# Kernel tuning notes

Measured on AMD Instinct MI355X. Metric: run time of the kernel, lower is better.

The kernel has to match this reference:

```python
import jax, jax.numpy as jnp
import numpy as np

B, R, IN_DIM = 32, 512, 1024
K, D = 4096, 256  # num_codebook_vectors, latent_dim
OUT_DIM = 1024
BETA = 0.25


def setup_inputs() -> dict:
    key = jax.random.key(0)
    ks = jax.random.split(key, 5)
    scale = 1.0 / K
    return {
        "z": jax.random.normal(ks[0], (B, R, IN_DIM), dtype=jnp.float32),
        "W_qa": jax.random.normal(ks[1], (IN_DIM, 2 * D), dtype=jnp.float32) * (IN_DIM ** -0.5),
        "b_qa": jnp.zeros((2 * D,), dtype=jnp.float32),
        "emb1": jax.random.uniform(ks[2], (K, D), dtype=jnp.float32, minval=-scale, maxval=scale),
        "emb2": jax.random.uniform(ks[3], (K, D), dtype=jnp.float32, minval=-scale, maxval=scale),
        "W_pq": jax.random.normal(ks[4], (2 * D, OUT_DIM), dtype=jnp.float32) * ((2 * D) ** -0.5),
        "b_pq": jnp.zeros((OUT_DIM,), dtype=jnp.float32),
    }


def _vq(z_h, emb):
    # z_h: [B, R, D], emb: [K, D]
    zf = z_h.reshape(-1, D)  # [N, D]
    # squared-distance matrix via GEMM: [N, K]
    d = (jnp.sum(zf * zf, axis=1, keepdims=True)
         + jnp.sum(emb * emb, axis=1)
         - 2.0 * zf @ emb.T)
    idx = jnp.argmin(d, axis=1)  # [N]
    z_q = emb[idx].reshape(z_h.shape)  # gather [B, R, D]
    enc_loss = jnp.mean((jax.lax.stop_gradient(z_q) - z_h) ** 2, axis=-1)
    code_loss = jnp.mean((z_q - jax.lax.stop_gradient(z_h)) ** 2, axis=-1)
    loss = enc_loss + BETA * code_loss  # [B, R]
    z_q_st = z_h + jax.lax.stop_gradient(z_q - z_h)  # straight-through
    return z_q_st, idx.reshape(z_h.shape[:2]), loss


def reference(z, W_qa, b_qa, emb1, emb2, W_pq, b_pq):
    h = z @ W_qa + b_qa  # [B, R, 2D]
    z1, z2 = h[..., :D], h[..., D:]
    zq1, idx1, loss1 = _vq(z1, emb1)
    zq2, idx2, loss2 = _vq(z2, emb2)
    loss = 0.5 * (loss1 + loss2)  # [B, R]
    z_q = jnp.concatenate([zq1, zq2], axis=-1) @ W_pq + b_pq  # [B, R, OUT_DIM]
    return z_q, idx1, idx2, loss
```

## Files before the change

### kernel.cpp

```cpp
#include <hip/hip_runtime.h>
#include <cstdint>
#include <cstddef>

#define MROWS 16384
#define INDIM 1024
#define DD    256
#define TWO_D 512
#define KC    4096
#define OUTD  1024
#define NZQ   (MROWS * OUTD)

typedef short bfrag __attribute__((ext_vector_type(8)));
typedef float ffrag __attribute__((ext_vector_type(4)));

__device__ __forceinline__ ushort f2bf(float f) {
    uint u = __float_as_uint(f);
    return (ushort)((u + 0x7FFFu + ((u >> 16) & 1u)) >> 16);
}

#define GLD16(dst, src)                                                        \
    __builtin_amdgcn_global_load_lds(                                          \
        (const __attribute__((address_space(1))) unsigned int*)(src),          \
        (__attribute__((address_space(3))) unsigned int*)(dst), 16, 0, 0)

__global__ __launch_bounds__(256) void k_gemm1(const float* __restrict__ z,
                                               const float* __restrict__ Wqa,
                                               const float* __restrict__ bqa,
                                               float* __restrict__ h,
                                               ushort* __restrict__ hbf) {
    __shared__ float As[2][128][16];
    __shared__ float Bs[2][16][128];
    const int tid = threadIdx.x;
    const int l = tid & 63, w = tid >> 6;
    const int tx = tid & 15, ty = tid >> 4;
    const int rb = blockIdx.x * 128;
    const int cb = blockIdx.y * 128;

    float acc[8][8] = {};

    const int sA = 4 * ((l & 3) ^ ((l >> 4) & 3));
    const float* aA0 = z + (size_t)(rb + 32 * w + (l >> 2)) * INDIM + sA;
    const float* aA1 = aA0 + (size_t)16 * INDIM;
    const float* bB0 = Wqa + (size_t)(4 * w + (l >> 5)) * TWO_D + cb + (l & 31) * 4;
    const float* bB1 = bB0 + (size_t)2 * TWO_D;

#define STAGE(buf, k0)                                                         \
    do {                                                                       \
        GLD16(&As[buf][32 * w][0],      aA0 + (k0));                           \
        GLD16(&As[buf][32 * w + 16][0], aA1 + (k0));                           \
        GLD16(&Bs[buf][4 * w][0],       bB0 + (size_t)(k0) * TWO_D);           \
        GLD16(&Bs[buf][4 * w + 2][0],   bB1 + (size_t)(k0) * TWO_D);           \
    } while (0)

    STAGE(0, 0);
    __syncthreads();

    const int xk = ty & 3;
    for (int t = 0; t < 64; ++t) {
        const int cur = t & 1;
        if (t < 63) STAGE(cur ^ 1, (t + 1) * 16);
        #pragma unroll
        for (int q = 0; q < 4; ++q) {
            float fa[8][4];
            #pragma unroll
            for (int i = 0; i < 4; ++i) {
                *reinterpret_cast<float4*>(&fa[i][0]) =
                    *reinterpret_cast<const float4*>(&As[cur][ty * 4 + i][(q ^ xk) * 4]);
                *reinterpret_cast<float4*>(&fa[4 + i][0]) =
                    *reinterpret_cast<const float4*>(&As[cur][64 + ty * 4 + i][(q ^ xk) * 4]);
            }
            #pragma unroll
            for (int c = 0; c < 4; ++c) {
                const int kk = q * 4 + c;
                float4 b0 = *reinterpret_cast<const float4*>(&Bs[cur][kk][tx * 4]);
                float4 b1 = *reinterpret_cast<const float4*>(&Bs[cur][kk][64 + tx * 4]);
                float bv[8] = {b0.x, b0.y, b0.z, b0.w, b1.x, b1.y, b1.z, b1.w};
                #pragma unroll
                for (int i = 0; i < 8; ++i)
                    #pragma unroll
                    for (int j = 0; j < 8; ++j)
                        acc[i][j] = fmaf(fa[i][c], bv[j], acc[i][j]);
            }
        }
        __syncthreads();
    }
#undef STAGE

    #pragma unroll
    for (int i = 0; i < 8; ++i) {
        const int row = rb + ((i < 4) ? (ty * 4 + i) : (64 + ty * 4 + i - 4));
        #pragma unroll
        for (int jh = 0; jh < 2; ++jh) {
            const int col = cb + jh * 64 + tx * 4;
            float v0 = acc[i][jh * 4 + 0] + bqa[col + 0];
            float v1 = acc[i][jh * 4 + 1] + bqa[col + 1];
            float v2 = acc[i][jh * 4 + 2] + bqa[col + 2];
            float v3 = acc[i][jh * 4 + 3] + bqa[col + 3];
            float4 vf = {v0, v1, v2, v3};
            *reinterpret_cast<float4*>(&h[(size_t)row * TWO_D + col]) = vf;
            ushort u[4] = {f2bf(v0), f2bf(v1), f2bf(v2), f2bf(v3)};
            *reinterpret_cast<uint2*>(&hbf[(size_t)row * TWO_D + col]) =
                *reinterpret_cast<uint2*>(u);
        }
    }
}

__global__ __launch_bounds__(256) void k_rnorm(const float* __restrict__ h,
                                               float* __restrict__ Rn) {
    const int wave = threadIdx.x >> 6;
    const int lane = threadIdx.x & 63;
    const int item = blockIdx.x * 4 + wave;
    const int row  = item & (MROWS - 1);
    const int half = item >> 14;
    float4 v = *reinterpret_cast<const float4*>(&h[(size_t)row * TWO_D + half * DD + lane * 4]);
    float s = v.x * v.x + v.y * v.y + v.z * v.z + v.w * v.w;
    #pragma unroll
    for (int off = 32; off; off >>= 1) s += __shfl_down(s, off, 64);
    if (lane == 0) Rn[half * MROWS + row] = s;
}

__global__ __launch_bounds__(256) void k_cvt(const float* __restrict__ e1,
                                             const float* __restrict__ e2,
                                             const float* __restrict__ Wpq,
                                             ushort* __restrict__ ebf,
                                             ushort* __restrict__ wbfT) {
    const int b = blockIdx.x;
    if (b < 2048) {
        const size_t v = ((size_t)b * 256 + threadIdx.x) * 4;
        const size_t half = (size_t)KC * DD;
        const float* src = (v < half) ? (e1 + v) : (e2 + (v - half));
        float4 f = *reinterpret_cast<const float4*>(src);
        ebf[v + 0] = f2bf(f.x); ebf[v + 1] = f2bf(f.y);
        ebf[v + 2] = f2bf(f.z); ebf[v + 3] = f2bf(f.w);
    } else {
        const int e = ((b - 2048) * 256 + threadIdx.x) * 4;
        const int k = e >> 10, c = e & 1023;
        float4 f = *reinterpret_cast<const float4*>(&Wpq[e]);
        wbfT[(size_t)(c + 0) * TWO_D + k] = f2bf(f.x);
        wbfT[(size_t)(c + 1) * TWO_D + k] = f2bf(f.y);
        wbfT[(size_t)(c + 2) * TWO_D + k] = f2bf(f.z);
        wbfT[(size_t)(c + 3) * TWO_D + k] = f2bf(f.w);
    }
}

__global__ __launch_bounds__(256) void k_score_mfma(const ushort* __restrict__ hbf,
                                                    const ushort* __restrict__ ebf,
                                                    uint* __restrict__ cand) {
    __shared__ ushort Ab[2][4][128][8];
    __shared__ ushort Bb[2][4][128][8];
    const int tid = threadIdx.x;
    const int l = tid & 63, w = tid >> 6;
    const int rb    = blockIdx.x * 128;
    const int cbcol = blockIdx.y * 128;
    const int cbk   = blockIdx.z;
    const ushort* hb = hbf + cbk * DD;
    const ushort* eb = ebf + (size_t)cbk * KC * DD;

    const int ry = (w & 1) * 64;
    const int cy = (w >> 1) * 64;

    const int koct = (w ^ ((l >> 1) & 3)) * 8;
    const ushort* aS0 = hb + (size_t)(rb + l) * TWO_D + koct;
    const ushort* aS1 = hb + (size_t)(rb + 64 + l) * TWO_D + koct;
    const ushort* bS0 = eb + (size_t)(cbcol + l) * DD + koct;
    const ushort* bS1 = eb + (size_t)(cbcol + 64 + l) * DD + koct;

#define SSTAGE(buf, k0)                                                        \
    do {                                                                       \
        GLD16(&Ab[buf][w][0][0],  aS0 + (k0));                                 \
        GLD16(&Ab[buf][w][64][0], aS1 + (k0));                                 \
        GLD16(&Bb[buf][w][0][0],  bS0 + (k0));                                 \
        GLD16(&Bb[buf][w][64][0], bS1 + (k0));                                 \
    } while (0)

    ffrag acc[4][4];
    #pragma unroll
    for (int i = 0; i < 4; ++i)
        #pragma unroll
        for (int j = 0; j < 4; ++j)
            acc[i][j] = (ffrag){0.f, 0.f, 0.f, 0.f};

    SSTAGE(0, 0);
    __syncthreads();

    const int q = l >> 4, li = l & 15;
    for (int c = 0; c < 8; ++c) {
        const int cur = c & 1;
        if (c < 7) SSTAGE(cur ^ 1, (c + 1) * 32);
        bfrag afr[4], bfr[4];
        #pragma unroll
        for (int rf = 0; rf < 4; ++rf) {
            const int r = ry + rf * 16 + li;
            afr[rf] = *reinterpret_cast<const bfrag*>(&Ab[cur][q ^ ((r >> 1) & 3)][r][0]);
        }
        #pragma unroll
        for (int cf = 0; cf < 4; ++cf) {
            const int cc = cy + cf * 16 + li;
            bfr[cf] = *reinterpret_cast<const bfrag*>(&Bb[cur][q ^ ((cc >> 1) & 3)][cc][0]);
        }
        #pragma unroll
        for (int rf = 0; rf < 4; ++rf)
            #pragma unroll
            for (int cf = 0; cf < 4; ++cf)
                acc[rf][cf] = __builtin_amdgcn_mfma_f32_16x16x32_bf16(afr[rf], bfr[cf],
                                                                      acc[rf][cf], 0, 0, 0);
        __syncthreads();
    }
#undef SSTAGE

    const int seg = blockIdx.y * 2 + (w >> 1);
    #pragma unroll
    for (int rf = 0; rf < 4; ++rf) {
        #pragma unroll
        for (int reg = 0; reg < 4; ++reg) {
            const int row = rb + ry + rf * 16 + q * 4 + reg;
            uint k1 = 0, k2 = 0;
            #pragma unroll
            for (int cf = 0; cf < 4; ++cf) {
                float v = acc[rf][cf][reg];
                const int code = cbcol + cy + cf * 16 + li;
                uint u = __float_as_uint(v);
                u ^= (0x80000000u | (uint)((int)u >> 31));
                const uint key = (u & 0xFFFFF000u) | (uint)code;
                if (key > k1) { k2 = k1; k1 = key; }
                else if (key > k2) { k2 = key; }
            }
            #pragma unroll
            for (int m = 1; m < 16; m <<= 1) {
                uint o1 = __shfl_xor((int)k1, m, 64);
                uint o2 = __shfl_xor((int)k2, m, 64);
                uint n1 = k1 > o1 ? k1 : o1;
                uint lo = k1 > o1 ? o1 : k1;
                uint hi2 = k2 > o2 ? k2 : o2;
                k2 = lo > hi2 ? lo : hi2;
                k1 = n1;
            }
            if (li == 0) {
                const size_t base = ((size_t)(cbk * 64 + seg) * MROWS + row) * 2;
                cand[base] = k1; cand[base + 1] = k2;
            }
        }
    }
}

__global__ __launch_bounds__(256) void k_reduce(const uint* __restrict__ cand,
                                                const float* __restrict__ h,
                                                const float* __restrict__ emb1,
                                                const float* __restrict__ emb2,
                                                const float* __restrict__ Rn,
                                                float* __restrict__ dout_idx) {
    const int tid = threadIdx.x;
    const int l = tid & 63, w = tid >> 6;
    const int item = blockIdx.x * 4 + w;
    const int cb  = item >> 14;
    const int row = item & (MROWS - 1);

    const size_t base = ((size_t)(cb * 64 + l) * MROWS + row) * 2;
    uint k1 = cand[base], k2 = cand[base + 1];

    uint mykey = 0;
    #pragma unroll
    for (int t = 0; t < 8; ++t) {
        uint m = k1 > k2 ? k1 : k2;
        #pragma unroll
        for (int off = 1; off < 64; off <<= 1) {
            uint o = __shfl_xor((int)m, off, 64);
            m = m > o ? m : o;
        }
        if (k1 == m) k1 = 0; else if (k2 == m) k2 = 0;
        if (l == t) mykey = m;
    }

    float dd = INFINITY; int code = 0x7fffffff;
    if (l < 8) {
        code = (int)(mykey & 0xFFFu);
        const float* hr = h + (size_t)row * TWO_D + cb * DD;
        const float* er = (cb ? emb2 : emb1) + (size_t)code * DD;
        float M = 0.f;
        for (int d = 0; d < DD; ++d) M = fmaf(hr[d], er[d], M);
        dd = Rn[cb * MROWS + row] - 2.0f * M;
    }
    #pragma unroll
    for (int off = 1; off < 8; off <<= 1) {
        float od = __shfl_xor(dd, off, 64);
        int   oc = __shfl_xor(code, off, 64);
        if (od < dd || (od == dd && oc < code)) { dd = od; code = oc; }
    }
    if (l == 0) dout_idx[cb * MROWS + row] = (float)code;
}

__global__ __launch_bounds__(256) void k_loss(const float* __restrict__ h,
                                              const float* __restrict__ emb1,
                                              const float* __restrict__ emb2,
                                              const float* __restrict__ idxf,
                                              float* __restrict__ dout_loss) {
    __shared__ float red[4];
    const int r = blockIdx.x;
    const int d = threadIdx.x;
    const int ia = (int)idxf[r];
    const int ib = (int)idxf[MROWS + r];
    float e1 = emb1[(size_t)ia * DD + d];
    float e2 = emb2[(size_t)ib * DD + d];
    float h1 = h[(size_t)r * TWO_D + d];
    float h2 = h[(size_t)r * TWO_D + DD + d];
    float d1 = e1 - h1, d2 = e2 - h2;
    float p = d1 * d1 + d2 * d2;
    #pragma unroll
    for (int off = 32; off; off >>= 1) p += __shfl_down(p, off, 64);
    const int lane = d & 63, wv = d >> 6;
    if (lane == 0) red[wv] = p;
    __syncthreads();
    if (d == 0) {
        float s = red[0] + red[1] + red[2] + red[3];
        dout_loss[r] = s * (0.625f / 256.0f);
    }
}

__global__ __launch_bounds__(256) void k_gemm2m(const ushort* __restrict__ ebf,
                                                const ushort* __restrict__ wbfT,
                                                const float* __restrict__ idxf,
                                                const float* __restrict__ bpq,
                                                float* __restrict__ out) {
    __shared__ ushort Ab[2][4][128][8];
    __shared__ ushort Bb[2][4][128][8];
    const int tid = threadIdx.x;
    const int l = tid & 63, w = tid >> 6;
    const int rb    = blockIdx.x * 128;
    const int cbcol = blockIdx.y * 128;
    const int ry = (w & 1) * 64;
    const int cy = (w >> 1) * 64;
    const ushort* e1 = ebf;
    const ushort* e2 = ebf + (size_t)KC * DD;

    const int ia0 = (int)idxf[rb + l];
    const int ia1 = (int)idxf[rb + 64 + l];
    const int ib0 = (int)idxf[MROWS + rb + l];
    const int ib1 = (int)idxf[MROWS + rb + 64 + l];

    const int koct = (w ^ ((l >> 1) & 3)) * 8;
    const ushort* aA0 = e1 + (size_t)ia0 * DD + koct;
    const ushort* aA1 = e1 + (size_t)ia1 * DD + koct;
    const ushort* aB0 = e2 + (size_t)ib0 * DD + koct;
    const ushort* aB1 = e2 + (size_t)ib1 * DD + koct;
    const ushort* bS0 = wbfT + (size_t)(cbcol + l) * TWO_D + koct;
    const ushort* bS1 = wbfT + (size_t)(cbcol + 64 + l) * TWO_D + koct;

#define GSTAGE(buf, c)                                                         \
    do {                                                                       \
        const int cbs_ = (c) >> 3;                                             \
        const int ka_  = ((c) * 32) & 255;                                     \
        GLD16(&Ab[buf][w][0][0],  (cbs_ ? aB0 : aA0) + ka_);                   \
        GLD16(&Ab[buf][w][64][0], (cbs_ ? aB1 : aA1) + ka_);                   \
        GLD16(&Bb[buf][w][0][0],  bS0 + (c) * 32);                             \
        GLD16(&Bb[buf][w][64][0], bS1 + (c) * 32);                             \
    } while (0)

    ffrag acc[4][4];
    #pragma unroll
    for (int i = 0; i < 4; ++i)
        #pragma unroll
        for (int j = 0; j < 4; ++j)
            acc[i][j] = (ffrag){0.f, 0.f, 0.f, 0.f};

    GSTAGE(0, 0);
    __syncthreads();

    const int q = l >> 4, li = l & 15;
    for (int c = 0; c < 16; ++c) {
        const int cur = c & 1;
        if (c < 15) GSTAGE(cur ^ 1, c + 1);
        bfrag afr[4], bfr[4];
        #pragma unroll
        for (int rf = 0; rf < 4; ++rf) {
            const int r = ry + rf * 16 + li;
            afr[rf] = *reinterpret_cast<const bfrag*>(&Ab[cur][q ^ ((r >> 1) & 3)][r][0]);
        }
        #pragma unroll
        for (int cf = 0; cf < 4; ++cf) {
            const int cc = cy + cf * 16 + li;
            bfr[cf] = *reinterpret_cast<const bfrag*>(&Bb[cur][q ^ ((cc >> 1) & 3)][cc][0]);
        }
        #pragma unroll
        for (int rf = 0; rf < 4; ++rf)
            #pragma unroll
            for (int cf = 0; cf < 4; ++cf)
                acc[rf][cf] = __builtin_amdgcn_mfma_f32_16x16x32_bf16(afr[rf], bfr[cf],
                                                                      acc[rf][cf], 0, 0, 0);
        __syncthreads();
    }
#undef GSTAGE

    #pragma unroll
    for (int rf = 0; rf < 4; ++rf) {
        #pragma unroll
        for (int reg = 0; reg < 4; ++reg) {
            const int row = rb + ry + rf * 16 + q * 4 + reg;
            #pragma unroll
            for (int cf = 0; cf < 4; ++cf) {
                const int col = cbcol + cy + cf * 16 + li;
                out[(size_t)row * OUTD + col] = acc[rf][cf][reg] + bpq[col];
            }
        }
    }
}

extern "C" void kernel_launch(void* const* d_in, const int* in_sizes, int n_in,
                              void* d_out, int out_size, void* d_ws, size_t ws_size,
                              hipStream_t stream) {
    const float* z    = (const float*)d_in[0];
    const float* Wqa  = (const float*)d_in[1];
    const float* bqa  = (const float*)d_in[2];
    const float* emb1 = (const float*)d_in[3];
    const float* emb2 = (const float*)d_in[4];
    const float* Wpq  = (const float*)d_in[5];
    const float* bpq  = (const float*)d_in[6];
    float* out = (float*)d_out;

    const size_t H = (size_t)MROWS * TWO_D;
    float*  hbuf = (float*)d_ws;
    float*  Rn   = hbuf + H;
    ushort* hbf  = (ushort*)(Rn + 2 * MROWS);
    ushort* ebf  = hbf + H;
    ushort* wbfT = ebf + 2 * (size_t)KC * DD;
    uint*   cand = (uint*)(wbfT + (size_t)OUTD * TWO_D);

    float* dout_idx  = out + NZQ;
    float* dout_loss = out + NZQ + 2 * MROWS;

    k_gemm1<<<dim3(128, 4), 256, 0, stream>>>(z, Wqa, bqa, hbuf, hbf);
    k_rnorm<<<8192, 256, 0, stream>>>(hbuf, Rn);
    k_cvt<<<2560, 256, 0, stream>>>(emb1, emb2, Wpq, ebf, wbfT);
    k_score_mfma<<<dim3(128, 32, 2), 256, 0, stream>>>(hbf, ebf, cand);
    k_reduce<<<8192, 256, 0, stream>>>(cand, hbuf, emb1, emb2, Rn, dout_idx);
    k_loss<<<16384, 256, 0, stream>>>(hbuf, emb1, emb2, dout_idx, dout_loss);
    k_gemm2m<<<dim3(128, 8), 256, 0, stream>>>(ebf, wbfT, dout_idx, bpq, out);
}
```

Baseline: 618.1 us.

## Store candidate keys row-contiguous and reduce eight rows per wavefront

The candidate buffer is laid out so the 128 keys for one (codebook,row) pair are contiguous instead of strided by MROWS. The reduce kernel now handles 8 rows per wavefront, with each 8-lane group loading 16 keys through vector loads. It does a local max plus a 3-step shuffle instead of a 6-step shuffle over 64 lanes, and the rescoring dot product uses float4 loads. This cuts strided uncoalesced reads and shuffle work, and drops the block count by 8x, at the cost of higher register use for the 16-key array.

```diff
diff --git a/kernel.cpp b/kernel.cpp
--- a/kernel.cpp
+++ b/kernel.cpp
@@ -236,7 +236,7 @@
                 k1 = n1;
             }
             if (li == 0) {
-                const size_t base = ((size_t)(cbk * 64 + seg) * MROWS + row) * 2;
+                const size_t base = ((size_t)cbk * MROWS + row) * 128 + seg * 2;
                 cand[base] = k1; cand[base + 1] = k2;
             }
         }
@@ -251,42 +251,55 @@
                                                 float* __restrict__ dout_idx) {
     const int tid = threadIdx.x;
     const int l = tid & 63, w = tid >> 6;
-    const int item = blockIdx.x * 4 + w;
+    const int g = l & 7;
+    const int item = blockIdx.x * 32 + w * 8 + (l >> 3);
     const int cb  = item >> 14;
     const int row = item & (MROWS - 1);
 
-    const size_t base = ((size_t)(cb * 64 + l) * MROWS + row) * 2;
-    uint k1 = cand[base], k2 = cand[base + 1];
+    const uint* kp = cand + (size_t)item * 128 + g * 16;
+    uint k[16];
+    #pragma unroll
+    for (int j = 0; j < 4; ++j) {
+        uint4 v = *reinterpret_cast<const uint4*>(kp + j * 4);
+        k[j * 4 + 0] = v.x; k[j * 4 + 1] = v.y;
+        k[j * 4 + 2] = v.z; k[j * 4 + 3] = v.w;
+    }
 
     uint mykey = 0;
     #pragma unroll
     for (int t = 0; t < 8; ++t) {
-        uint m = k1 > k2 ? k1 : k2;
-        #pragma unroll
-        for (int off = 1; off < 64; off <<= 1) {
-            uint o = __shfl_xor((int)m, off, 64);
-            m = m > o ? m : o;
-        }
-        if (k1 == m) k1 = 0; else if (k2 == m) k2 = 0;
-        if (l == t) mykey = m;
-    }
-
-    float dd = INFINITY; int code = 0x7fffffff;
-    if (l < 8) {
-        code = (int)(mykey & 0xFFFu);
-        const float* hr = h + (size_t)row * TWO_D + cb * DD;
-        const float* er = (cb ? emb2 : emb1) + (size_t)code * DD;
-        float M = 0.f;
-        for (int d = 0; d < DD; ++d) M = fmaf(hr[d], er[d], M);
-        dd = Rn[cb * MROWS + row] - 2.0f * M;
-    }
+        uint m = k[0];
+        #pragma unroll
+        for (int j = 1; j < 16; ++j) m = k[j] > m ? k[j] : m;
+        #pragma unroll
+        for (int off = 1; off < 8; off <<= 1) {
+            uint o = (uint)__shfl_xor((int)m, off, 64);
+            m = o > m ? o : m;
+        }
+        #pragma unroll
+        for (int j = 0; j < 16; ++j) k[j] = (k[j] == m) ? 0u : k[j];
+        if (g == t) mykey = m;
+    }
+
+    const int code = (int)(mykey & 0xFFFu);
+    const float* hr = h + (size_t)row * TWO_D + cb * DD;
+    const float* er = (cb ? emb2 : emb1) + (size_t)code * DD;
+    float M = 0.f;
+    for (int d = 0; d < DD; d += 4) {
+        float4 a = *reinterpret_cast<const float4*>(hr + d);
+        float4 b = *reinterpret_cast<const float4*>(er + d);
+        M = fmaf(a.x, b.x, M); M = fmaf(a.y, b.y, M);
+        M = fmaf(a.z, b.z, M); M = fmaf(a.w, b.w, M);
+    }
+    float dd = Rn[cb * MROWS + row] - 2.0f * M;
+    int c2 = code;
     #pragma unroll
     for (int off = 1; off < 8; off <<= 1) {
         float od = __shfl_xor(dd, off, 64);
-        int   oc = __shfl_xor(code, off, 64);
-        if (od < dd || (od == dd && oc < code)) { dd = od; code = oc; }
-    }
-    if (l == 0) dout_idx[cb * MROWS + row] = (float)code;
+        int   oc = __shfl_xor(c2, off, 64);
+        if (od < dd || (od == dd && oc < c2)) { dd = od; c2 = oc; }
+    }
+    if (g == 0) dout_idx[cb * MROWS + row] = (float)c2;
 }
 
 __global__ __launch_bounds__(256) void k_loss(const float* __restrict__ h,
@@ -431,7 +444,7 @@
     k_rnorm<<<8192, 256, 0, stream>>>(hbuf, Rn);
     k_cvt<<<2560, 256, 0, stream>>>(emb1, emb2, Wpq, ebf, wbfT);
     k_score_mfma<<<dim3(128, 32, 2), 256, 0, stream>>>(hbf, ebf, cand);
-    k_reduce<<<8192, 256, 0, stream>>>(cand, hbuf, emb1, emb2, Rn, dout_idx);
+    k_reduce<<<1024, 256, 0, stream>>>(cand, hbuf, emb1, emb2, Rn, dout_idx);
     k_loss<<<16384, 256, 0, stream>>>(hbuf, emb1, emb2, dout_idx, dout_loss);
     k_gemm2m<<<dim3(128, 8), 256, 0, stream>>>(ebf, wbfT, dout_idx, bpq, out);
 }
```

Result: faster. 543.1 us (-12.1%).
